# Performance work log

Measured on AMD Instinct MI355X. Metric: run time of the kernel, lower is better.

Reference implementation:

```python
import jax, jax.numpy as jnp
import numpy as np

B, L, NV = 16, 512, 64
D = 512
PATCH_LEN, STRIDE, PADDING = 16, 8, 8
N_PATCH = (L - PATCH_LEN) // STRIDE + 2  # 64
PRED = 192
MEM = 8192
TOPK = 8
NHEAD = 4
NORM_CONST = 0.4
HEAD_NF = D * N_PATCH


def _pos_emb(n, d):
    pos = np.arange(n)[:, None].astype(np.float32)
    div = np.exp(np.arange(0, d, 2).astype(np.float32) * (-np.log(10000.0) / d))
    pe = np.zeros((n, d), np.float32)
    pe[:, 0::2] = np.sin(pos * div)
    pe[:, 1::2] = np.cos(pos * div)
    return jnp.asarray(pe)

POS = _pos_emb(N_PATCH, D)


def gelu(x):
    return jax.nn.gelu(x, approximate=False)  # torch nn.GELU default = exact erf


def setup_inputs() -> dict:
    key = jax.random.key(0)
    ks = jax.random.split(key, 16)
    s = lambda i, shape, scale=0.02: jax.random.normal(ks[i], shape, jnp.float32) * scale
    return dict(
        x_enc=jax.random.normal(ks[0], (B, L, NV), jnp.float32),
        W_val=s(1, (PATCH_LEN, D), 0.05),
        mem_bank=s(2, (MEM, D), 1.0),
        W_m1=s(3, (D, 2 * D)), b_m1=jnp.zeros((2 * D,), jnp.float32),
        W_m2=s(4, (2 * D, D)), b_m2=jnp.zeros((D,), jnp.float32),
        W_q=s(5, (D, D)), b_q=jnp.zeros((D,), jnp.float32),
        W_k=s(6, (D, D)), b_k=jnp.zeros((D,), jnp.float32),
        W_v=s(7, (D, D)), b_v=jnp.zeros((D,), jnp.float32),
        W_o=s(8, (D, D)), b_o=jnp.zeros((D,), jnp.float32),
        W_g1=s(9, (2 * D, D)), b_g1=jnp.zeros((D,), jnp.float32),
        W_g2=s(10, (D, 2)), b_g2=jnp.zeros((2,), jnp.float32),
        W_h=s(11, (HEAD_NF, PRED)), b_h=jnp.zeros((PRED,), jnp.float32),
        W_f1=s(12, (PRED, 2 * PRED)), b_f1=jnp.zeros((2 * PRED,), jnp.float32),
        W_f2=s(13, (2 * PRED, PRED)), b_f2=jnp.zeros((PRED,), jnp.float32),
    )


def reference(x_enc, W_val, mem_bank, W_m1, b_m1, W_m2, b_m2,
              W_q, b_q, W_k, b_k, W_v, b_v, W_o, b_o,
              W_g1, b_g1, W_g2, b_g2, W_h, b_h, W_f1, b_f1, W_f2, b_f2):
    # instance normalization over the time axis (means detached in torch)
    means = jax.lax.stop_gradient(jnp.mean(x_enc, axis=1, keepdims=True))
    xc = x_enc - means
    stdev = jnp.sqrt(jnp.var(xc, axis=1, keepdims=True) + 1e-5) / NORM_CONST
    x = xc / stdev                                              # [B, L, NV]

    # patch embedding: replication pad at end, unfold, linear + sinusoidal pos
    xt = jnp.transpose(x, (0, 2, 1))                            # [B, NV, L]
    xt = jnp.concatenate([xt, jnp.repeat(xt[..., -1:], PADDING, axis=-1)], axis=-1)
    win = (jnp.arange(N_PATCH) * STRIDE)[:, None] + jnp.arange(PATCH_LEN)  # [N, P]
    patches = xt[..., win].reshape(B * NV, N_PATCH, PATCH_LEN)  # [BN, N, P]
    emb = patches @ W_val + POS                                 # [BN, N, D]

    # local memory: mean-pooled query -> matmul similarity -> top-k gather -> MLP
    qflat = jnp.mean(emb, axis=1)                               # [BN, D]
    sim = qflat @ mem_bank.T                                    # [BN, MEM]
    _, idx = jax.lax.top_k(sim, TOPK)                           # [BN, K]
    retr = mem_bank[idx]                                        # [BN, K, D]
    h = gelu(retr @ W_m1 + b_m1) @ W_m2 + b_m2
    local = jnp.mean(h, axis=1, keepdims=True) + emb            # [BN, N, D]

    # global memory: multihead self-attention (4 heads, batch_first)
    dh = D // NHEAD
    heads = lambda t: t.reshape(B * NV, N_PATCH, NHEAD, dh).transpose(0, 2, 1, 3)
    q = heads(emb @ W_q + b_q)
    k = heads(emb @ W_k + b_k)
    v = heads(emb @ W_v + b_v)
    att = jax.nn.softmax(jnp.einsum('bhqd,bhkd->bhqk', q, k) / jnp.sqrt(jnp.float32(dh)), axis=-1)
    glob = jnp.einsum('bhqk,bhkd->bhqd', att, v).transpose(0, 2, 1, 3).reshape(B * NV, N_PATCH, D)
    glob = glob @ W_o + b_o                                     # [BN, N, D]

    # gated fusion of local/global memory
    comb = jnp.concatenate([local, glob], axis=-1)              # [BN, N, 2D]
    gate = jax.nn.softmax(gelu(comb @ W_g1 + b_g1) @ W_g2 + b_g2, axis=-1)
    mem = gate[..., 0:1] * local + gate[..., 1:2] * glob        # [BN, N, D]

    # flatten -> memory head -> fusion layer with residual
    flat = mem.reshape(B * NV, HEAD_NF)
    mh = (flat @ W_h + b_h).reshape(B, NV, PRED)
    pred = gelu(gelu(mh @ W_f1 + b_f1) @ W_f2 + b_f2) + mh
    pred = jnp.transpose(pred, (0, 2, 1))                       # [B, PRED, NV]

    # denormalize
    return pred * stdev + means
```

## Files before the change

kernel.cpp:

```cpp
#include <hip/hip_runtime.h>
#include <stdint.h>

#define DEV __device__ __forceinline__

typedef uint16_t u16;
typedef __bf16 bf16x8 __attribute__((ext_vector_type(8)));
typedef float f32x4 __attribute__((ext_vector_type(4)));
typedef u16 u16x8 __attribute__((ext_vector_type(8)));

DEV float bf2f(u16 v) { return __uint_as_float(((uint32_t)v) << 16); }
DEV u16 f2bf(float f) {
  uint32_t u = __float_as_uint(f);
  u += 0x7fffu + ((u >> 16) & 1u);
  return (u16)(u >> 16);
}
DEV float gelu_f(float x) { return 0.5f * x * (1.0f + erff(x * 0.7071067811865475f)); }

DEV void gload_lds16(const u16* g, u16* l) {
  __builtin_amdgcn_global_load_lds(
      (const __attribute__((address_space(1))) void*)g,
      (__attribute__((address_space(3))) void*)l, 16, 0, 0);
}

struct __align__(16) Scratch {
  float POSb[64 * 512];
  float meanv[1024];
  float stdv[1024];
  float mh[1024 * 192];
  int idxB[8192];
  float qflat[1024 * 512];
  float gatel[65536 * 2];
  float bqkv[1536];
  u16 hmeanB[1024 * 512];
  u16 gmeanB[1024 * 1024];
  u16 WqkvT[1536 * 512];
  u16 WoT[512 * 512];
  u16 Wm1T[1024 * 512];
  u16 Wm2T[512 * 1024];
  u16 Wg1T[512 * 1024];
  u16 WhT[256 * 32768];
  u16 memdupB[8192 * 1536];
  u16 embh[65536 * 512];
  u16 qkvb[65536 * 1536];
};
__device__ Scratch g_s;

__global__ __launch_bounds__(256) void zerof_kernel(float* __restrict__ p, int n) {
  int t = blockIdx.x * 256 + threadIdx.x;
  if (t < n) p[t] = 0.f;
}
__global__ __launch_bounds__(256) void zerou8_kernel(u16* __restrict__ p, int n8) {
  int t = blockIdx.x * 256 + threadIdx.x;
  if (t < n8) *(u16x8*)(p + (long)t * 8) = (u16x8)0;
}
__global__ __launch_bounds__(256) void biasqkv_kernel(const float* __restrict__ bq,
                                                      const float* __restrict__ bk,
                                                      const float* __restrict__ bv,
                                                      float* __restrict__ o) {
  int t = blockIdx.x * 256 + threadIdx.x;
  o[t] = t < 512 ? bq[t] : (t < 1024 ? bk[t - 512] : bv[t - 1024]);
}

__global__ __launch_bounds__(256) void pos_kernel(float* __restrict__ POS) {
  int n = blockIdx.x;
  int i = threadIdx.x;
  float div = expf((float)(2 * i) * (-9.210340371976184f / 512.0f));
  float arg = (float)n * div;
  POS[n * 512 + 2 * i] = sinf(arg);
  POS[n * 512 + 2 * i + 1] = cosf(arg);
}

__global__ __launch_bounds__(256) void stats_kernel(const float* __restrict__ x_enc,
                                                    float* __restrict__ meanv,
                                                    float* __restrict__ stdv) {
  int b = blockIdx.x;
  int v = threadIdx.x & 63;
  int g = threadIdx.x >> 6;
  float s = 0.f, s2 = 0.f;
  for (int l = g; l < 512; l += 4) {
    float x = x_enc[((long)b * 512 + l) * 64 + v];
    s += x; s2 += x * x;
  }
  __shared__ float sh[2][4][64];
  sh[0][g][v] = s; sh[1][g][v] = s2;
  __syncthreads();
  if (g == 0) {
    s = sh[0][0][v] + sh[0][1][v] + sh[0][2][v] + sh[0][3][v];
    s2 = sh[1][0][v] + sh[1][1][v] + sh[1][2][v] + sh[1][3][v];
    float mu = s * (1.f / 512.f);
    float var = s2 * (1.f / 512.f) - mu * mu;
    meanv[b * 64 + v] = mu;
    stdv[b * 64 + v] = sqrtf(var + 1e-5f) * 2.5f;
  }
}

__global__ __launch_bounds__(256) void transpose_kernel(const float* __restrict__ in,
                                                        u16* __restrict__ out, int R, int C) {
  __shared__ u16 t[32][33];
  int bx = blockIdx.x * 32;
  int by = blockIdx.y * 32;
  int tx = threadIdx.x & 31, ty = threadIdx.x >> 5;
  for (int i = ty; i < 32; i += 8) t[i][tx] = f2bf(in[(long)(by + i) * C + bx + tx]);
  __syncthreads();
  for (int i = ty; i < 32; i += 8) out[(long)(bx + i) * R + by + tx] = t[tx][i];
}

__global__ __launch_bounds__(256) void emb_kernel(const float* __restrict__ x_enc,
                                                  const float* __restrict__ W_val,
                                                  const float* __restrict__ POS,
                                                  const float* __restrict__ meanv,
                                                  const float* __restrict__ stdv,
                                                  u16* __restrict__ embh,
                                                  float* __restrict__ qflat) {
  int bn = blockIdx.x;
  int b = bn >> 6, v = bn & 63;
  int tid = threadIdx.x;
  __shared__ __align__(16) float wv[16 * 512];
  __shared__ __align__(16) float pt[64 * 16];
  for (int i = tid; i < 8192; i += 256) wv[i] = W_val[i];
  float mu = meanv[bn];
  float inv = 1.f / stdv[bn];
  for (int i = tid; i < 1024; i += 256) {
    int n = i >> 4, p = i & 15;
    int l = n * 8 + p; if (l > 511) l = 511;
    pt[i] = (x_enc[((long)b * 512 + l) * 64 + v] - mu) * inv;
  }
  __syncthreads();
  float qs0 = 0.f, qs1 = 0.f;
  int d0 = tid, d1 = tid + 256;
  for (int n = 0; n < 64; ++n) {
    float a0 = POS[n * 512 + d0], a1 = POS[n * 512 + d1];
#pragma unroll
    for (int p = 0; p < 16; ++p) {
      float pv = pt[n * 16 + p];
      a0 += pv * wv[p * 512 + d0];
      a1 += pv * wv[p * 512 + d1];
    }
    long base = ((long)bn * 64 + n) * 512;
    embh[base + d0] = f2bf(a0);
    embh[base + d1] = f2bf(a1);
    qs0 += a0; qs1 += a1;
  }
  qflat[(long)bn * 512 + d0] = qs0 * (1.f / 64.f);
  qflat[(long)bn * 512 + d1] = qs1 * (1.f / 64.f);
}

__global__ __launch_bounds__(256) void qsplit_kernel(const float* __restrict__ qflat,
                                                     u16* __restrict__ qsC) {
  int t = blockIdx.x * 256 + threadIdx.x;
  int bn = t >> 6, d8 = (t & 63) * 8;
  const float* src = qflat + (long)bn * 512 + d8;
  u16x8 hi, lo;
#pragma unroll
  for (int z = 0; z < 8; ++z) {
    float q = src[z];
    u16 h = f2bf(q);
    hi[z] = h;
    lo[z] = f2bf(q - bf2f(h));
  }
  long base = (long)bn * 1536 + d8;
  *(u16x8*)(qsC + base) = hi;
  *(u16x8*)(qsC + base + 512) = lo;
  *(u16x8*)(qsC + base + 1024) = hi;
}

__global__ __launch_bounds__(256) void memdup_kernel(const float* __restrict__ mb,
                                                     u16* __restrict__ md) {
  int t = blockIdx.x * 256 + threadIdx.x;
  int n = t >> 6, k8 = (t & 63) * 8;
  const float* src = mb + (long)n * 512 + k8;
  u16x8 hi, lo;
#pragma unroll
  for (int z = 0; z < 8; ++z) {
    float m = src[z];
    u16 h = f2bf(m);
    hi[z] = h;
    lo[z] = f2bf(m - bf2f(h));
  }
  long base = (long)n * 1536 + k8;
  *(u16x8*)(md + base) = hi;
  *(u16x8*)(md + base + 512) = hi;
  *(u16x8*)(md + base + 1024) = lo;
}

template <int EPI>
__global__ __launch_bounds__(256) void gemm_nt(const u16* __restrict__ Ag,
                                               const u16* __restrict__ Bt,
                                               const float* __restrict__ bias,
                                               void* __restrict__ C,
                                               int lda, int ldb, int K, int Nreal, int ldc,
                                               int nT, long zstride) {
  __shared__ __align__(16) u16 smem[2 * 128 * 64];
  u16* As = smem;
  u16* Bs = smem + 8192;
  const int tid = threadIdx.x;
  const int id = blockIdx.x;
  const int xcd = id & 7;
  const int kk = id >> 3;
  const long bm = (long)((kk / nT) * 8 + xcd) * 128;
  const long bnn = (long)(kk % nT) * 128;
  const long koff = (long)blockIdx.z * K;
  const int lane = tid & 63;
  const int w = tid >> 6;
  const int wm = (w & 1) * 64;
  const int wn = (w >> 1) * 64;
  const int r16 = lane & 15;
  const int q4 = lane >> 4;

  f32x4 acc[4][4] = {};

  const u16* ap[4];
  const u16* bp[4];
  u16* al[4];
  u16* bl[4];
#pragma unroll
  for (int j = 0; j < 4; ++j) {
    int cid = (j * 4 + w) * 64 + lane;
    int r = cid >> 3;
    int g = (cid & 7) ^ (r & 7);
    ap[j] = Ag + (bm + r) * lda + koff + g * 8;
    bp[j] = Bt + (bnn + r) * ldb + koff + g * 8;
    al[j] = As + cid * 8;
    bl[j] = Bs + cid * 8;
  }

  for (int k0 = 0; k0 < K; k0 += 64) {
#pragma unroll
    for (int j = 0; j < 4; ++j) gload_lds16(ap[j] + k0, al[j]);
#pragma unroll
    for (int j = 0; j < 4; ++j) gload_lds16(bp[j] + k0, bl[j]);
    __syncthreads();
#pragma unroll
    for (int sub = 0; sub < 2; ++sub) {
      const int gg = q4 + sub * 4;
      bf16x8 av[4], bv[4];
#pragma unroll
      for (int i = 0; i < 4; ++i) {
        int r = wm + i * 16 + r16;
        av[i] = *reinterpret_cast<const bf16x8*>(As + (r * 8 + (gg ^ (r & 7))) * 8);
      }
#pragma unroll
      for (int j2 = 0; j2 < 4; ++j2) {
        int r = wn + j2 * 16 + r16;
        bv[j2] = *reinterpret_cast<const bf16x8*>(Bs + (r * 8 + (gg ^ (r & 7))) * 8);
      }
#pragma unroll
      for (int i = 0; i < 4; ++i)
#pragma unroll
        for (int j2 = 0; j2 < 4; ++j2)
          acc[i][j2] = __builtin_amdgcn_mfma_f32_16x16x32_bf16(av[i], bv[j2], acc[i][j2], 0, 0, 0);
    }
    __syncthreads();
  }

  if (EPI == 3) {
    float* Cz = (float*)C + (long)blockIdx.z * zstride;
    float* epf = (float*)smem + w * 2048;
#pragma unroll
    for (int half = 0; half < 2; ++half) {
#pragma unroll
      for (int i = 0; i < 2; ++i)
#pragma unroll
        for (int j = 0; j < 4; ++j)
#pragma unroll
          for (int r = 0; r < 4; ++r)
            epf[(i * 16 + q4 * 4 + r) * 64 + ((j * 16 + r16) ^ (q4 << 4))] =
                acc[half * 2 + i][j][r];
      __syncthreads();
#pragma unroll
      for (int v2 = 0; v2 < 8; ++v2) {
        int idx = v2 * 64 + lane;
        int row = idx >> 4, c4 = (idx & 15) * 4;
        int c4s = c4 ^ (((row >> 2) & 3) << 4);
        f32x4 vec = *(const f32x4*)(epf + row * 64 + c4s);
        long grow = bm + wm + half * 32 + row;
        int gcol = (int)bnn + wn + c4;
        if (gcol < Nreal) *(f32x4*)(Cz + grow * (long)ldc + gcol) = vec;
      }
      __syncthreads();
    }
  } else {
    u16* ep = smem + w * 4096;
    float bcol[4];
#pragma unroll
    for (int j = 0; j < 4; ++j) bcol[j] = bias[bnn + wn + j * 16 + r16];
#pragma unroll
    for (int i = 0; i < 4; ++i)
#pragma unroll
      for (int j = 0; j < 4; ++j)
#pragma unroll
        for (int r = 0; r < 4; ++r) {
          float v = acc[i][j][r] + bcol[j];
          if (EPI == 1) v = gelu_f(v);
          ep[(i * 16 + q4 * 4 + r) * 64 + ((j * 16 + r16) ^ (q4 << 4))] = f2bf(v);
        }
    __syncthreads();
#pragma unroll
    for (int v2 = 0; v2 < 8; ++v2) {
      int row = v2 * 8 + (lane >> 3);
      int c8 = (lane & 7) * 8;
      int c8s = c8 ^ (((row >> 2) & 3) << 4);
      u16x8 vec = *(const u16x8*)(ep + row * 64 + c8s);
      long grow = bm + wm + row;
      int gcol = (int)bnn + wn + c8;
      if (gcol < Nreal) *(u16x8*)((u16*)C + grow * (long)ldc + gcol) = vec;
    }
  }
}

DEV bool better(float v1, int i1, float v2, int i2) {
  return v1 > v2 || (v1 == v2 && i1 < i2);
}
__global__ __launch_bounds__(256) void topk_kernel(const float* __restrict__ sim,
                                                   int* __restrict__ idxout) {
  const int bn = blockIdx.x;
  const int tid = threadIdx.x;
  const float* row = sim + (long)bn * 8192;
  float bv[8]; int bi[8];
#pragma unroll
  for (int r = 0; r < 8; ++r) { bv[r] = -3.0e38f; bi[r] = 0x7fffffff; }
  for (int n = tid; n < 8192; n += 256) {
    float v = row[n];
    if (better(v, n, bv[7], bi[7])) {
      bv[7] = v; bi[7] = n;
      for (int r = 7; r > 0; --r) {
        if (!better(bv[r], bi[r], bv[r - 1], bi[r - 1])) break;
        float tv = bv[r]; bv[r] = bv[r - 1]; bv[r - 1] = tv;
        int ti = bi[r]; bi[r] = bi[r - 1]; bi[r - 1] = ti;
      }
    }
  }
  __shared__ float lv[256 * 8];
  __shared__ int li[256 * 8];
#pragma unroll
  for (int r = 0; r < 8; ++r) { lv[tid * 8 + r] = bv[r]; li[tid * 8 + r] = bi[r]; }
  __syncthreads();
  for (int step = 128; step >= 1; step >>= 1) {
    if (tid < step) {
      float av[8], xv[8]; int ai[8], xi[8];
#pragma unroll
      for (int r = 0; r < 8; ++r) {
        av[r] = lv[tid * 8 + r]; ai[r] = li[tid * 8 + r];
        xv[r] = lv[(tid + step) * 8 + r]; xi[r] = li[(tid + step) * 8 + r];
      }
      int ia = 0, ib = 0;
      float mv[8]; int mi[8];
#pragma unroll
      for (int r = 0; r < 8; ++r) {
        if (better(av[ia], ai[ia], xv[ib], xi[ib])) { mv[r] = av[ia]; mi[r] = ai[ia]; ++ia; }
        else { mv[r] = xv[ib]; mi[r] = xi[ib]; ++ib; }
      }
#pragma unroll
      for (int r = 0; r < 8; ++r) { lv[tid * 8 + r] = mv[r]; li[tid * 8 + r] = mi[r]; }
    }
    __syncthreads();
  }
  if (tid < 8) idxout[bn * 8 + tid] = li[tid];
}

__global__ __launch_bounds__(256) void gather_kernel(const float* __restrict__ mb,
                                                     const int* __restrict__ idx,
                                                     u16* __restrict__ retrB) {
  int t = blockIdx.x * 256 + threadIdx.x;
  int m = t >> 6;
  int c8 = (t & 63) * 8;
  long r = idx[m];
  if (r < 0) r = 0;
  if (r > 8191) r = 8191;
  const float* src = mb + r * 512 + c8;
  u16x8 o;
#pragma unroll
  for (int z = 0; z < 8; ++z) o[z] = f2bf(src[z]);
  *(u16x8*)(retrB + (long)m * 512 + c8) = o;
}

__global__ __launch_bounds__(256) void gmean_kernel(const u16* __restrict__ hid,
                                                    u16* __restrict__ gmeanB) {
  int t = blockIdx.x * 256 + threadIdx.x;
  int bn = t >> 7, j8 = (t & 127) * 8;
  float s[8] = {};
#pragma unroll
  for (int k = 0; k < 8; ++k) {
    u16x8 v = *(const u16x8*)(hid + (long)(bn * 8 + k) * 1024 + j8);
#pragma unroll
    for (int z = 0; z < 8; ++z) s[z] += bf2f(v[z]);
  }
  u16x8 o;
#pragma unroll
  for (int z = 0; z < 8; ++z) o[z] = f2bf(s[z] * 0.125f);
  *(u16x8*)(gmeanB + (long)bn * 1024 + j8) = o;
}

__global__ __launch_bounds__(256) void attn_kernel(u16* __restrict__ qkvb) {
  __shared__ __align__(16) u16 smem[26752];
  u16* Qs = smem;
  u16* Ks = smem + 8704;
  float* ss = (float*)(smem + 8704);
  u16* ps = smem;
  u16* Os = smem;
  u16* Vb = smem + 17408;
  float* red = (float*)(smem + 25728);
  const int bn = blockIdx.x, h = blockIdx.y;
  const int tid = threadIdx.x;
  const int lane = tid & 63, w = tid >> 6;
  const int r16 = lane & 15, q4 = lane >> 4;
  const long base = (long)bn * 64 * 1536 + h * 128;

  for (int c = tid; c < 1024; c += 256) {
    int r = c >> 4, c8 = (c & 15) * 8;
    u16x8 vq = *(const u16x8*)(qkvb + base + (long)r * 1536 + c8);
    u16x8 vk = *(const u16x8*)(qkvb + base + (long)r * 1536 + 512 + c8);
    u16x8 vv = *(const u16x8*)(qkvb + base + (long)r * 1536 + 1024 + c8);
    *(u16x8*)(Qs + r * 136 + c8) = vq;
    *(u16x8*)(Ks + r * 136 + c8) = vk;
    int kt = r >> 5, q4t = (r >> 3) & 3, e = r & 7;
    int nt = c8 >> 4, rb = c8 & 15;
    int vbase = (nt * 2 + kt) * 520 + (q4t * 16 + rb) * 8 + e;
#pragma unroll
    for (int z = 0; z < 8; ++z) Vb[vbase + z * 8] = vv[z];
  }
  __syncthreads();

  const int m0 = w * 16;
  f32x4 accS[4] = {};
#pragma unroll
  for (int k0 = 0; k0 < 128; k0 += 32) {
    bf16x8 av = *(const bf16x8*)(Qs + (m0 + r16) * 136 + k0 + q4 * 8);
#pragma unroll
    for (int j = 0; j < 4; ++j) {
      bf16x8 bvf = *(const bf16x8*)(Ks + (j * 16 + r16) * 136 + k0 + q4 * 8);
      accS[j] = __builtin_amdgcn_mfma_f32_16x16x32_bf16(av, bvf, accS[j], 0, 0, 0);
    }
  }
  __syncthreads();
  const float scale = 0.08838834764831845f;
#pragma unroll
  for (int j = 0; j < 4; ++j)
#pragma unroll
    for (int r = 0; r < 4; ++r)
      ss[(m0 + q4 * 4 + r) * 66 + j * 16 + r16] = accS[j][r] * scale;
  __syncthreads();

  {
    int r = tid >> 2, p = tid & 3;
    float* row = ss + r * 66 + p * 16;
    float mx = -3.0e38f;
#pragma unroll
    for (int c2 = 0; c2 < 16; ++c2) mx = fmaxf(mx, row[c2]);
    red[r * 4 + p] = mx;
    __syncthreads();
    float m4 = fmaxf(fmaxf(red[r * 4], red[r * 4 + 1]),
                     fmaxf(red[r * 4 + 2], red[r * 4 + 3]));
    float s = 0.f;
#pragma unroll
    for (int c2 = 0; c2 < 16; ++c2) {
      float e = expf(row[c2] - m4);
      row[c2] = e;
      s += e;
    }
    red[256 + r * 4 + p] = s;
    __syncthreads();
    float inv = 1.f / (red[256 + r * 4] + red[256 + r * 4 + 1] +
                       red[256 + r * 4 + 2] + red[256 + r * 4 + 3]);
    u16x8 o0, o1;
#pragma unroll
    for (int z = 0; z < 8; ++z) {
      o0[z] = f2bf(row[z] * inv);
      o1[z] = f2bf(row[8 + z] * inv);
    }
    *(u16x8*)(ps + r * 72 + p * 16) = o0;
    *(u16x8*)(ps + r * 72 + p * 16 + 8) = o1;
  }
  __syncthreads();

  bf16x8 av0 = *(const bf16x8*)(ps + (m0 + r16) * 72 + q4 * 8);
  bf16x8 av1 = *(const bf16x8*)(ps + (m0 + r16) * 72 + 32 + q4 * 8);
  __syncthreads();
#pragma unroll
  for (int nt = 0; nt < 8; ++nt) {
    f32x4 accO = {};
    bf16x8 bv0 = *(const bf16x8*)(Vb + (nt * 2 + 0) * 520 + lane * 8);
    bf16x8 bv1 = *(const bf16x8*)(Vb + (nt * 2 + 1) * 520 + lane * 8);
    accO = __builtin_amdgcn_mfma_f32_16x16x32_bf16(av0, bv0, accO, 0, 0, 0);
    accO = __builtin_amdgcn_mfma_f32_16x16x32_bf16(av1, bv1, accO, 0, 0, 0);
#pragma unroll
    for (int r = 0; r < 4; ++r) {
      int i = m0 + q4 * 4 + r;
      int col = nt * 16 + r16;
      Os[i * 128 + (col ^ (q4 << 4))] = f2bf(accO[r]);
    }
  }
  __syncthreads();
#pragma unroll
  for (int z = 0; z < 4; ++z) {
    int idx = z * 256 + tid;
    int row = idx >> 4, c8 = (idx & 15) * 8;
    int c8s = c8 ^ (((row >> 2) & 3) << 4);
    u16x8 vec = *(const u16x8*)(Os + row * 128 + c8s);
    *(u16x8*)(qkvb + base + (long)row * 1536 + c8) = vec;
  }
}

__global__ __launch_bounds__(256) void local_kernel(u16* __restrict__ embh,
                                                    const u16* __restrict__ hmeanB) {
  long t = (long)blockIdx.x * 256 + threadIdx.x;
  long e8 = t * 8;
  long m = e8 >> 9;
  int d = (int)(e8 & 511);
  int bn = (int)(m >> 6);
  u16x8 a = *(const u16x8*)(embh + e8);
  u16x8 b = *(const u16x8*)(hmeanB + (long)bn * 512 + d);
  u16x8 o;
#pragma unroll
  for (int z = 0; z < 8; ++z) o[z] = f2bf(bf2f(a[z]) + bf2f(b[z]));
  *(u16x8*)(embh + e8) = o;
}

__global__ __launch_bounds__(256) void gemm_cat(const u16* __restrict__ A1,
                                                const u16* __restrict__ A2,
                                                const u16* __restrict__ Bt,
                                                const float* __restrict__ bias,
                                                const float* __restrict__ W_g2,
                                                float* __restrict__ gatel,
                                                int lda1, int lda2, int nT) {
  __shared__ __align__(16) u16 smem[2 * 128 * 64];
  u16* As = smem;
  u16* Bs = smem + 8192;
  const int tid = threadIdx.x;
  const int id = blockIdx.x;
  const int xcd = id & 7;
  const int kk = id >> 3;
  const long bm = (long)((kk / nT) * 8 + xcd) * 128;
  const long bnn = (long)(kk % nT) * 128;
  const int lane = tid & 63;
  const int w = tid >> 6;
  const int wm = (w & 1) * 64;
  const int wn = (w >> 1) * 64;
  const int r16 = lane & 15;
  const int q4 = lane >> 4;

  f32x4 acc[4][4] = {};

  const u16* ap1[4];
  const u16* ap2[4];
  const u16* bp[4];
  u16* al[4];
  u16* bl[4];
#pragma unroll
  for (int j = 0; j < 4; ++j) {
    int cid = (j * 4 + w) * 64 + lane;
    int r = cid >> 3;
    int g = (cid & 7) ^ (r & 7);
    ap1[j] = A1 + (bm + r) * lda1 + g * 8;
    ap2[j] = A2 + (bm + r) * lda2 + g * 8;
    bp[j] = Bt + (bnn + r) * 1024 + g * 8;
    al[j] = As + cid * 8;
    bl[j] = Bs + cid * 8;
  }

  for (int k0 = 0; k0 < 1024; k0 += 64) {
    if (k0 < 512) {
#pragma unroll
      for (int j = 0; j < 4; ++j) gload_lds16(ap1[j] + k0, al[j]);
    } else {
#pragma unroll
      for (int j = 0; j < 4; ++j) gload_lds16(ap2[j] + (k0 - 512), al[j]);
    }
#pragma unroll
    for (int j = 0; j < 4; ++j) gload_lds16(bp[j] + k0, bl[j]);
    __syncthreads();
#pragma unroll
    for (int sub = 0; sub < 2; ++sub) {
      const int gg = q4 + sub * 4;
      bf16x8 av[4], bv[4];
#pragma unroll
      for (int i = 0; i < 4; ++i) {
        int r = wm + i * 16 + r16;
        av[i] = *reinterpret_cast<const bf16x8*>(As + (r * 8 + (gg ^ (r & 7))) * 8);
      }
#pragma unroll
      for (int j2 = 0; j2 < 4; ++j2) {
        int r = wn + j2 * 16 + r16;
        bv[j2] = *reinterpret_cast<const bf16x8*>(Bs + (r * 8 + (gg ^ (r & 7))) * 8);
      }
#pragma unroll
      for (int i = 0; i < 4; ++i)
#pragma unroll
        for (int j2 = 0; j2 < 4; ++j2)
          acc[i][j2] = __builtin_amdgcn_mfma_f32_16x16x32_bf16(av[i], bv[j2], acc[i][j2], 0, 0, 0);
    }
    __syncthreads();
  }

  float bcol[4], w0[4], w1[4];
#pragma unroll
  for (int j = 0; j < 4; ++j) {
    int gc = (int)bnn + wn + j * 16 + r16;
    bcol[j] = bias[gc];
    w0[j] = W_g2[gc * 2];
    w1[j] = W_g2[gc * 2 + 1];
  }
#pragma unroll
  for (int i = 0; i < 4; ++i)
#pragma unroll
    for (int r = 0; r < 4; ++r) {
      float a0 = 0.f, a1 = 0.f;
#pragma unroll
      for (int j = 0; j < 4; ++j) {
        float h = gelu_f(acc[i][j][r] + bcol[j]);
        a0 += h * w0[j];
        a1 += h * w1[j];
      }
#pragma unroll
      for (int off = 1; off < 16; off <<= 1) {
        a0 += __shfl_xor(a0, off);
        a1 += __shfl_xor(a1, off);
      }
      if (r16 == 0) {
        long row = bm + wm + i * 16 + q4 * 4 + r;
        atomicAdd(&gatel[row * 2], a0);
        atomicAdd(&gatel[row * 2 + 1], a1);
      }
    }
}

__global__ __launch_bounds__(256) void memc_kernel(u16* __restrict__ embh,
                                                   const u16* __restrict__ qkvb,
                                                   const float* __restrict__ gatel,
                                                   const float* __restrict__ b_g2) {
  long t = (long)blockIdx.x * 256 + threadIdx.x;
  long e8 = t * 8;
  long m = e8 >> 9;
  int d = (int)(e8 & 511);
  float l0 = gatel[m * 2] + b_g2[0];
  float l1 = gatel[m * 2 + 1] + b_g2[1];
  float mx = fmaxf(l0, l1);
  float e0 = expf(l0 - mx), e1 = expf(l1 - mx);
  float inv = 1.f / (e0 + e1);
  float g0 = e0 * inv, g1 = e1 * inv;
  u16x8 loc = *(const u16x8*)(embh + e8);
  u16x8 gl = *(const u16x8*)(qkvb + m * 1536 + 512 + d);
  u16x8 o;
#pragma unroll
  for (int z = 0; z < 8; ++z) o[z] = f2bf(g0 * bf2f(loc[z]) + g1 * bf2f(gl[z]));
  *(u16x8*)(embh + e8) = o;
}

__global__ __launch_bounds__(256) void fusion_kernel(const float* __restrict__ mh16,
                                                     const float* __restrict__ b_h,
                                                     const float* __restrict__ W_f1,
                                                     const float* __restrict__ b_f1,
                                                     const float* __restrict__ W_f2,
                                                     const float* __restrict__ b_f2,
                                                     const float* __restrict__ meanv,
                                                     const float* __restrict__ stdv,
                                                     float* __restrict__ out) {
  int bn = blockIdx.x;
  int tid = threadIdx.x;
  __shared__ float mrow[192];
  __shared__ float h1[384];
  if (tid < 192) {
    float a = b_h[tid];
#pragma unroll
    for (int z = 0; z < 16; ++z) a += mh16[(long)z * 196608 + (long)bn * 192 + tid];
    mrow[tid] = a;
  }
  __syncthreads();
  for (int j = tid; j < 384; j += 256) {
    float a = b_f1[j];
    for (int i = 0; i < 192; ++i) a += mrow[i] * W_f1[i * 384 + j];
    h1[j] = gelu_f(a);
  }
  __syncthreads();
  if (tid < 192) {
    float a = b_f2[tid];
    for (int j = 0; j < 384; ++j) a += h1[j] * W_f2[j * 192 + tid];
    float o = gelu_f(a) + mrow[tid];
    int b = bn >> 6, v = bn & 63;
    out[((long)b * 192 + tid) * 64 + v] = o * stdv[bn] + meanv[bn];
  }
}

extern "C" void kernel_launch(void* const* d_in, const int* in_sizes, int n_in,
                              void* d_out, int out_size, void* d_ws, size_t ws_size,
                              hipStream_t stream) {
  (void)in_sizes; (void)n_in; (void)out_size; (void)d_ws; (void)ws_size;
  const float* x_enc = (const float*)d_in[0];
  const float* W_val = (const float*)d_in[1];
  const float* mem_bank = (const float*)d_in[2];
  const float* W_m1 = (const float*)d_in[3];
  const float* b_m1 = (const float*)d_in[4];
  const float* W_m2 = (const float*)d_in[5];
  const float* b_m2 = (const float*)d_in[6];
  const float* W_q = (const float*)d_in[7];
  const float* b_q = (const float*)d_in[8];
  const float* W_k = (const float*)d_in[9];
  const float* b_k = (const float*)d_in[10];
  const float* W_v = (const float*)d_in[11];
  const float* b_v = (const float*)d_in[12];
  const float* W_o = (const float*)d_in[13];
  const float* b_o = (const float*)d_in[14];
  const float* W_g1 = (const float*)d_in[15];
  const float* b_g1 = (const float*)d_in[16];
  const float* W_g2 = (const float*)d_in[17];
  const float* b_g2 = (const float*)d_in[18];
  const float* W_h = (const float*)d_in[19];
  const float* b_h = (const float*)d_in[20];
  const float* W_f1 = (const float*)d_in[21];
  const float* b_f1 = (const float*)d_in[22];
  const float* W_f2 = (const float*)d_in[23];
  const float* b_f2 = (const float*)d_in[24];

  void* sp = nullptr;
  hipGetSymbolAddress(&sp, HIP_SYMBOL(g_s));
  Scratch* S = (Scratch*)sp;
  float* simB = (float*)S->qkvb;
  u16* qsC = S->qkvb + (size_t)16 * 1024 * 1024;
  u16* retrB = S->qkvb + (size_t)18 * 1024 * 1024;
  u16* hiddenB = S->qkvb + (size_t)24 * 1024 * 1024;
  float* mh16 = (float*)S->qkvb;

  pos_kernel<<<64, 256, 0, stream>>>(S->POSb);
  stats_kernel<<<16, 256, 0, stream>>>(x_enc, S->meanv, S->stdv);
  zerof_kernel<<<512, 256, 0, stream>>>(S->gatel, 65536 * 2);
  zerou8_kernel<<<1024, 256, 0, stream>>>(S->WhT + (size_t)192 * 32768, 64 * 32768 / 8);
  biasqkv_kernel<<<6, 256, 0, stream>>>(b_q, b_k, b_v, S->bqkv);
  transpose_kernel<<<dim3(16, 16), 256, 0, stream>>>(W_q, S->WqkvT, 512, 512);
  transpose_kernel<<<dim3(16, 16), 256, 0, stream>>>(W_k, S->WqkvT + 512 * 512, 512, 512);
  transpose_kernel<<<dim3(16, 16), 256, 0, stream>>>(W_v, S->WqkvT + 2 * 512 * 512, 512, 512);
  transpose_kernel<<<dim3(16, 16), 256, 0, stream>>>(W_o, S->WoT, 512, 512);
  transpose_kernel<<<dim3(32, 16), 256, 0, stream>>>(W_m1, S->Wm1T, 512, 1024);
  transpose_kernel<<<dim3(16, 32), 256, 0, stream>>>(W_m2, S->Wm2T, 1024, 512);
  transpose_kernel<<<dim3(16, 32), 256, 0, stream>>>(W_g1, S->Wg1T, 1024, 512);
  transpose_kernel<<<dim3(6, 1024), 256, 0, stream>>>(W_h, S->WhT, 32768, 192);
  memdup_kernel<<<2048, 256, 0, stream>>>(mem_bank, S->memdupB);

  emb_kernel<<<1024, 256, 0, stream>>>(x_enc, W_val, S->POSb, S->meanv, S->stdv,
                                       S->embh, S->qflat);
  qsplit_kernel<<<256, 256, 0, stream>>>(S->qflat, qsC);
  gemm_nt<3><<<512, 256, 0, stream>>>(qsC, S->memdupB, nullptr, simB,
                                      1536, 1536, 1536, 8192, 8192, 64, 0L);
  topk_kernel<<<1024, 256, 0, stream>>>(simB, S->idxB);
  gather_kernel<<<2048, 256, 0, stream>>>(mem_bank, S->idxB, retrB);
  gemm_nt<1><<<512, 256, 0, stream>>>(retrB, S->Wm1T, b_m1, hiddenB,
                                      512, 512, 512, 1024, 1024, 8, 0L);
  gmean_kernel<<<512, 256, 0, stream>>>(hiddenB, S->gmeanB);
  gemm_nt<0><<<32, 256, 0, stream>>>(S->gmeanB, S->Wm2T, b_m2, S->hmeanB,
                                     1024, 1024, 1024, 512, 512, 4, 0L);
  gemm_nt<0><<<6144, 256, 0, stream>>>(S->embh, S->WqkvT, S->bqkv, S->qkvb,
                                       512, 512, 512, 1536, 1536, 12, 0L);
  local_kernel<<<16384, 256, 0, stream>>>(S->embh, S->hmeanB);
  attn_kernel<<<dim3(1024, 4), 256, 0, stream>>>(S->qkvb);
  gemm_nt<0><<<2048, 256, 0, stream>>>(S->qkvb, S->WoT, b_o, S->qkvb + 512,
                                       1536, 512, 512, 512, 1536, 4, 0L);
  gemm_cat<<<2048, 256, 0, stream>>>(S->embh, S->qkvb + 512, S->Wg1T, b_g1,
                                     W_g2, S->gatel, 512, 1536, 4);
  memc_kernel<<<16384, 256, 0, stream>>>(S->embh, S->qkvb, S->gatel, b_g2);
  gemm_nt<3><<<dim3(16, 1, 16), 256, 0, stream>>>(S->embh, S->WhT, nullptr, mh16,
                                                  32768, 32768, 2048, 192, 192, 2,
                                                  196608L);
  fusion_kernel<<<1024, 256, 0, stream>>>(mh16, b_h, W_f1, b_f1, W_f2, b_f2,
                                          S->meanv, S->stdv, (float*)d_out);
}
```

Baseline: 1.008 ms.

## Fuse query split into embedding kernel and rework GEMM epilogue LDS layout

The embedding kernel now writes the hi/lo bf16-split mean query directly, so the separate qsplit kernel launch and the float qflat round trip are gone. The GEMM epilogues drop the XOR swizzle. The fp32 path uses a plain row layout, and the bf16 path stages 32 rows at a time in a smaller per-wave buffer padded to a 72-element stride. This is meant to cut launch overhead, global traffic and index arithmetic, but the unswizzled fp32 layout may cause LDS bank conflicts and the halved bf16 epilogue adds an extra barrier.

After: 1.093 ms. 1.08x slower.

```diff
diff --git a/kernel.cpp b/kernel.cpp
--- a/kernel.cpp
+++ b/kernel.cpp
@@ -111,7 +111,7 @@
                                                   const float* __restrict__ meanv,
                                                   const float* __restrict__ stdv,
                                                   u16* __restrict__ embh,
-                                                  float* __restrict__ qflat) {
+                                                  u16* __restrict__ qsC) {
   int bn = blockIdx.x;
   int b = bn >> 6, v = bn & 63;
   int tid = threadIdx.x;
@@ -141,27 +141,12 @@
     embh[base + d1] = f2bf(a1);
     qs0 += a0; qs1 += a1;
   }
-  qflat[(long)bn * 512 + d0] = qs0 * (1.f / 64.f);
-  qflat[(long)bn * 512 + d1] = qs1 * (1.f / 64.f);
-}
-
-__global__ __launch_bounds__(256) void qsplit_kernel(const float* __restrict__ qflat,
-                                                     u16* __restrict__ qsC) {
-  int t = blockIdx.x * 256 + threadIdx.x;
-  int bn = t >> 6, d8 = (t & 63) * 8;
-  const float* src = qflat + (long)bn * 512 + d8;
-  u16x8 hi, lo;
-#pragma unroll
-  for (int z = 0; z < 8; ++z) {
-    float q = src[z];
-    u16 h = f2bf(q);
-    hi[z] = h;
-    lo[z] = f2bf(q - bf2f(h));
-  }
-  long base = (long)bn * 1536 + d8;
-  *(u16x8*)(qsC + base) = hi;
-  *(u16x8*)(qsC + base + 512) = lo;
-  *(u16x8*)(qsC + base + 1024) = hi;
+  float q0 = qs0 * (1.f / 64.f), q1 = qs1 * (1.f / 64.f);
+  u16 h0 = f2bf(q0), l0 = f2bf(q0 - bf2f(h0));
+  u16 h1 = f2bf(q1), l1 = f2bf(q1 - bf2f(h1));
+  long qb = (long)bn * 1536;
+  qsC[qb + d0] = h0; qsC[qb + 512 + d0] = l0; qsC[qb + 1024 + d0] = h0;
+  qsC[qb + d1] = h1; qsC[qb + 512 + d1] = l1; qsC[qb + 1024 + d1] = h1;
 }
 
 __global__ __launch_bounds__(256) void memdup_kernel(const float* __restrict__ mb,
@@ -264,15 +249,13 @@
         for (int j = 0; j < 4; ++j)
 #pragma unroll
           for (int r = 0; r < 4; ++r)
-            epf[(i * 16 + q4 * 4 + r) * 64 + ((j * 16 + r16) ^ (q4 << 4))] =
-                acc[half * 2 + i][j][r];
+            epf[(i * 16 + q4 * 4 + r) * 64 + j * 16 + r16] = acc[half * 2 + i][j][r];
       __syncthreads();
 #pragma unroll
       for (int v2 = 0; v2 < 8; ++v2) {
         int idx = v2 * 64 + lane;
         int row = idx >> 4, c4 = (idx & 15) * 4;
-        int c4s = c4 ^ (((row >> 2) & 3) << 4);
-        f32x4 vec = *(const f32x4*)(epf + row * 64 + c4s);
+        f32x4 vec = *(const f32x4*)(epf + row * 64 + c4);
         long grow = bm + wm + half * 32 + row;
         int gcol = (int)bnn + wn + c4;
         if (gcol < Nreal) *(f32x4*)(Cz + grow * (long)ldc + gcol) = vec;
@@ -280,30 +263,33 @@
       __syncthreads();
     }
   } else {
-    u16* ep = smem + w * 4096;
+    u16* ep = smem + w * 2304;
     float bcol[4];
 #pragma unroll
     for (int j = 0; j < 4; ++j) bcol[j] = bias[bnn + wn + j * 16 + r16];
 #pragma unroll
-    for (int i = 0; i < 4; ++i)
-#pragma unroll
-      for (int j = 0; j < 4; ++j)
-#pragma unroll
-        for (int r = 0; r < 4; ++r) {
-          float v = acc[i][j][r] + bcol[j];
-          if (EPI == 1) v = gelu_f(v);
-          ep[(i * 16 + q4 * 4 + r) * 64 + ((j * 16 + r16) ^ (q4 << 4))] = f2bf(v);
-        }
-    __syncthreads();
-#pragma unroll
-    for (int v2 = 0; v2 < 8; ++v2) {
-      int row = v2 * 8 + (lane >> 3);
-      int c8 = (lane & 7) * 8;
-      int c8s = c8 ^ (((row >> 2) & 3) << 4);
-      u16x8 vec = *(const u16x8*)(ep + row * 64 + c8s);
-      long grow = bm + wm + row;
-      int gcol = (int)bnn + wn + c8;
-      if (gcol < Nreal) *(u16x8*)((u16*)C + grow * (long)ldc + gcol) = vec;
+    for (int half = 0; half < 2; ++half) {
+#pragma unroll
+      for (int i = 0; i < 2; ++i)
+#pragma unroll
+        for (int j = 0; j < 4; ++j)
+#pragma unroll
+          for (int r = 0; r < 4; ++r) {
+            float v = acc[half * 2 + i][j][r] + bcol[j];
+            if (EPI == 1) v = gelu_f(v);
+            ep[(i * 16 + q4 * 4 + r) * 72 + j * 16 + r16] = f2bf(v);
+          }
+      __syncthreads();
+#pragma unroll
+      for (int v2 = 0; v2 < 4; ++v2) {
+        int row = v2 * 8 + (lane >> 3);
+        int c8 = (lane & 7) * 8;
+        u16x8 vec = *(const u16x8*)(ep + row * 72 + c8);
+        long grow = bm + wm + half * 32 + row;
+        int gcol = (int)bnn + wn + c8;
+        if (gcol < Nreal) *(u16x8*)((u16*)C + grow * (long)ldc + gcol) = vec;
+      }
+      __syncthreads();
     }
   }
 }
@@ -736,8 +722,7 @@
   memdup_kernel<<<2048, 256, 0, stream>>>(mem_bank, S->memdupB);
 
   emb_kernel<<<1024, 256, 0, stream>>>(x_enc, W_val, S->POSb, S->meanv, S->stdv,
-                                       S->embh, S->qflat);
-  qsplit_kernel<<<256, 256, 0, stream>>>(S->qflat, qsC);
+                                       S->embh, qsC);
   gemm_nt<3><<<512, 256, 0, stream>>>(qsC, S->memdupB, nullptr, simB,
                                       1536, 1536, 1536, 8192, 8192, 64, 0L);
   topk_kernel<<<1024, 256, 0, stream>>>(simB, S->idxB);
```
